# Performance work log

Measured on AMD Instinct MI355X. Metric: run time of the kernel, lower is better.

Reference implementation:

```python
import jax, jax.numpy as jnp
import numpy as np

WAY = 5
TEMPERATURE = 0.2
TEMPERATURE_ATTN = 5.0
BN_EPS = 1e-5


def bn_apply(x, p):
    # p: (4, C) = gamma, beta, running_mean, running_var (eval-mode BatchNorm)
    g, b, m, v = p[0], p[1], p[2], p[3]
    sh = (1, -1) + (1,) * (x.ndim - 2)
    return (x - m.reshape(sh)) * (g.reshape(sh) / jnp.sqrt(v.reshape(sh) + BN_EPS)) + b.reshape(sh)


def conv3d(x, w, pad):
    return jax.lax.conv_general_dilated(
        x, w, (1, 1, 1), [(pad[0], pad[0]), (pad[1], pad[1]), (pad[2], pad[2])],
        dimension_numbers=('NCDHW', 'OIDHW', 'NCDHW'))


def sepconv4d(x, conv2_w, bn2, conv1_w, bn1, proj_w, bnp):
    # x: (b, c, u, v, h, w). conv2: (k,k,1) kernel over (u,v); conv1: (1,k,k) over (h,w).
    b, c, u, v, h, w = x.shape
    y = x.reshape(b, c, u, v, h * w)
    y = bn_apply(conv3d(y, conv2_w, (1, 1, 0)), bn2)
    y = jax.nn.relu(y)
    y = y.reshape(b, c, u * v, h, w)
    y = bn_apply(conv3d(y, conv1_w, (0, 1, 1)), bn1)
    # 1x1 projection (pointwise over channels) + BN
    y = jnp.einsum('oc,bcxhw->boxhw', proj_w, y)
    y = bn_apply(y, bnp)
    return y.reshape(b, -1, u, v, h, w)


def cca(x, c1, c2):
    def branch(z):
        z = sepconv4d(z, *c1)
        z = jax.nn.relu(z)
        z = sepconv4d(z, *c2)
        return z
    perm = (0, 1, 4, 5, 2, 3)
    return branch(x) + jnp.transpose(branch(jnp.transpose(x, perm)), perm)


def gaussian_normalize(x, axis, eps=1e-5):
    m = jnp.mean(x, axis=axis, keepdims=True)
    v = jnp.var(x, axis=axis, keepdims=True, ddof=1)  # torch.var is unbiased
    return (x - m) / jnp.sqrt(v + eps)


def setup_inputs() -> dict:
    key = jax.random.key(0)
    ks = jax.random.split(key, 16)

    def bn_params(k, c):
        k1, k2, k3, k4 = jax.random.split(k, 4)
        g = 1.0 + 0.1 * jax.random.normal(k1, (c,), jnp.float32)
        b = 0.1 * jax.random.normal(k2, (c,), jnp.float32)
        m = 0.1 * jax.random.normal(k3, (c,), jnp.float32)
        v = 1.0 + 0.1 * jax.random.uniform(k4, (c,), jnp.float32)
        return jnp.stack([g, b, m, v])

    return {
        'spt': jax.random.normal(ks[0], (1, 5, 640, 10, 10), jnp.float32),
        'qry': jax.random.normal(ks[1], (75, 640, 10, 10), jnp.float32),
        'w_1x1': jax.random.normal(ks[2], (64, 640), jnp.float32) * 0.04,
        'bn_1x1': bn_params(ks[3], 64),
        'c1_conv2_w': jax.random.normal(ks[4], (1, 1, 3, 3, 1), jnp.float32) * 0.33,
        'c1_bn2': bn_params(ks[5], 1),
        'c1_conv1_w': jax.random.normal(ks[6], (1, 1, 1, 3, 3), jnp.float32) * 0.33,
        'c1_bn1': bn_params(ks[7], 1),
        'c1_proj_w': jax.random.normal(ks[8], (16, 1), jnp.float32),
        'c1_bnp': bn_params(ks[9], 16),
        'c2_conv2_w': jax.random.normal(ks[10], (16, 16, 3, 3, 1), jnp.float32) * 0.083,
        'c2_bn2': bn_params(ks[11], 16),
        'c2_conv1_w': jax.random.normal(ks[12], (16, 16, 1, 3, 3), jnp.float32) * 0.083,
        'c2_bn1': bn_params(ks[13], 16),
        'c2_proj_w': jax.random.normal(ks[14], (1, 16), jnp.float32) * 0.25,
        'c2_bnp': bn_params(ks[15], 1),
    }


def reference(spt, qry, w_1x1, bn_1x1,
              c1_conv2_w, c1_bn2, c1_conv1_w, c1_bn1, c1_proj_w, c1_bnp,
              c2_conv2_w, c2_bn2, c2_conv1_w, c2_bn1, c2_proj_w, c2_bnp):
    s = spt[0]                                   # (way, C, H, W)
    s = s - s.mean(axis=1, keepdims=True)        # normalize_feature
    q = qry - qry.mean(axis=1, keepdims=True)

    def cca1x1(x):
        y = jnp.einsum('oc,bchw->bohw', w_1x1, x)
        return jax.nn.relu(bn_apply(y, bn_1x1))

    sf = cca1x1(s)
    qf = cca1x1(q)
    sf = sf / jnp.maximum(jnp.linalg.norm(sf, axis=1, keepdims=True), 1e-8)
    qf = qf / jnp.maximum(jnp.linalg.norm(qf, axis=1, keepdims=True), 1e-8)

    # 4D correlation (avoids the repeat-induced 6D blowup of the original)
    corr = jnp.einsum('ncij,qckl->qnijkl', sf, qf)  # (Q, way, Hs, Ws, Hq, Wq)
    Q, way, Hs, Ws, Hq, Wq = corr.shape

    c1 = (c1_conv2_w, c1_bn2, c1_conv1_w, c1_bn1, c1_proj_w, c1_bnp)
    c2 = (c2_conv2_w, c2_bn2, c2_conv1_w, c2_bn1, c2_proj_w, c2_bnp)
    corr = cca(corr.reshape(Q * way, 1, Hs, Ws, Hq, Wq), c1, c2)

    corr_s = corr.reshape(Q, way, Hs * Ws, Hq, Wq)
    corr_q = corr.reshape(Q, way, Hs, Ws, Hq * Wq)
    corr_s = gaussian_normalize(corr_s, axis=2)
    corr_q = gaussian_normalize(corr_q, axis=4)
    corr_s = jax.nn.softmax(corr_s / TEMPERATURE_ATTN, axis=2).reshape(Q, way, Hs, Ws, Hq, Wq)
    corr_q = jax.nn.softmax(corr_q / TEMPERATURE_ATTN, axis=4).reshape(Q, way, Hs, Ws, Hq, Wq)

    attn_s = corr_s.sum(axis=(4, 5))             # (Q, way, Hs, Ws)
    attn_q = corr_q.sum(axis=(2, 3))             # (Q, way, Hq, Wq)

    spt_att = (attn_s[:, :, None] * s[None]).mean(axis=(-1, -2))       # (Q, way, C)
    qry_att = (attn_q[:, :, None] * q[:, None]).mean(axis=(-1, -2))    # (Q, way, C)
    qry_pooled = q.mean(axis=(-1, -2))                                  # (Q, C)

    num = jnp.sum(spt_att * qry_att, axis=-1)
    den = (jnp.maximum(jnp.linalg.norm(spt_att, axis=-1), 1e-8) *
           jnp.maximum(jnp.linalg.norm(qry_att, axis=-1), 1e-8))
    sim = (num / den) / TEMPERATURE
    return sim, qry_pooled
```

## Files before the change

kernel.cpp:

```cpp
#include <hip/hip_runtime.h>


#define NITEM 375

#define OFF_XTS 0
#define OFF_XTQ 160000
#define OFF_MP  2560000
#define OFF_SF  2568000
#define OFF_QF  2600000
#define OFF_RA  3080000
#define OFF_RB  6830000
#define OFF_PRM 10655000

#define PK2F 232
#define PK1F 1512
#define WSUMF 2792
#define SCVF 2856
#define SHVF 2920
#define PKWF 2984

#define Y1S2     20480
#define Y1GAP    1600
#define Y1HSTR   17600
#define Y1SSTR   35200
#define Y1BASE   (Y1S2 + Y1GAP)
#define ZPB2     127680
#define Y2S2     127712
#define Y2HALF2  16128
#define LDS_TOTAL2 159968

typedef float f4v __attribute__((ext_vector_type(4)));
typedef float f32x4 __attribute__((ext_vector_type(4)));
typedef _Float16 half8v __attribute__((ext_vector_type(8)));
typedef __fp16 fp16x2 __attribute__((ext_vector_type(2)));
typedef unsigned int u32x4 __attribute__((ext_vector_type(4)));
typedef unsigned int u32x2 __attribute__((ext_vector_type(2)));

__device__ __forceinline__ unsigned int pkrtz(float a, float b) {
  union { fp16x2 h; unsigned int u; } cv;
  cv.h = __builtin_amdgcn_cvt_pkrtz(a, b);
  return cv.u;
}

__global__ __launch_bounds__(256) void k_prep(
    const float* __restrict__ w1x1,  const float* __restrict__ bn1x1,
    const float* __restrict__ c1c2w, const float* __restrict__ c1bn2,
    const float* __restrict__ c1c1w, const float* __restrict__ c1bn1,
    const float* __restrict__ c1pj,  const float* __restrict__ c1bnp,
    const float* __restrict__ c2c2w, const float* __restrict__ c2bn2,
    const float* __restrict__ c2c1w, const float* __restrict__ c2bn1,
    const float* __restrict__ c2pj,  const float* __restrict__ c2bnp,
    float* __restrict__ prm)
{
  const int t = threadIdx.x;
  const float eps = 1e-5f;

  for (int idx = t; idx < 144; idx += 256) {
    int ds = idx / 16, i = idx % 16;
    float spv = c2bnp[0] / sqrtf(c2bnp[3] + eps);
    float acc = 0.f;
    for (int o = 0; o < 16; ++o) {
      float s1 = c2bn1[o] / sqrtf(c2bn1[48 + o] + eps);
      acc += c2pj[o] * s1 * c2c1w[(o * 16 + i) * 9 + ds];
    }
    prm[idx] = spv * acc;
  }
  for (int i = t; i < 16; i += 256) {
    float s = c1bnp[i] / sqrtf(c1bnp[48 + i] + eps);
    prm[144 + i] = s * c1pj[i];
    prm[160 + i] = c1bnp[16 + i] - c1bnp[32 + i] * s;
  }
  for (int o = t; o < 16; o += 256) {
    float s = c2bn2[o] / sqrtf(c2bn2[48 + o] + eps);
    prm[176 + o] = s;
    prm[192 + o] = c2bn2[16 + o] - c2bn2[32 + o] * s;
  }
  for (int k = t; k < 9; k += 256) {
    prm[208 + k] = c1c2w[k];
    prm[217 + k] = c1c1w[k];
  }
  if (t == 0) {
    float S2 = c1bn2[0] / sqrtf(c1bn2[3] + eps);
    prm[226] = S2;
    prm[227] = c1bn2[1] - c1bn2[2] * S2;
    float S1 = c1bn1[0] / sqrtf(c1bn1[3] + eps);
    prm[228] = S1;
    prm[229] = c1bn1[1] - c1bn1[2] * S1;
    float spv = c2bnp[0] / sqrtf(c2bnp[3] + eps);
    float k0 = 0.f;
    for (int o = 0; o < 16; ++o) {
      float s1 = c2bn1[o] / sqrtf(c2bn1[48 + o] + eps);
      k0 += c2pj[o] * (c2bn1[16 + o] - c2bn1[32 + o] * s1);
    }
    prm[230] = spv * (k0 - c2bnp[2]) + c2bnp[1];
    prm[231] = 0.f;
  }
  for (int o = t; o < 64; o += 256) {
    float s = 0.f;
    for (int c = 0; c < 640; ++c) s += w1x1[o * 640 + c];
    prm[WSUMF + o] = s;
    float scv = bn1x1[o] / sqrtf(bn1x1[192 + o] + eps);
    prm[SCVF + o] = scv;
    prm[SHVF + o] = bn1x1[64 + o] - bn1x1[128 + o] * scv;
  }
  __syncthreads();

  _Float16* pk2 = (_Float16*)(prm + PK2F);
  for (int idx = t; idx < 2560; idx += 256) {
    int c = idx >> 9, rem = idx & 511;
    int ln = rem >> 3, j = rem & 7;
    int o = ln & 15, qq = ln >> 4;
    int tap = 2 * c + (qq >> 1);
    int i = (qq & 1) * 8 + j;
    float v = (tap < 9) ? c2c2w[(o * 16 + i) * 9 + tap] : 0.f;
    pk2[idx] = (_Float16)v;
  }
  _Float16* pk1 = (_Float16*)(prm + PK1F);
  for (int idx = t; idx < 2560; idx += 256) {
    int c = idx >> 9, rem = idx & 511;
    int ln = rem >> 3, j = rem & 7;
    int m = ln & 15, qq = ln >> 4;
    int k = c * 32 + qq * 8 + j;
    int tp = k >> 4, i = k & 15;
    float v = (m == 0 && tp < 9) ? prm[tp * 16 + i] : 0.f;
    pk1[idx] = (_Float16)v;
  }
}

__global__ __launch_bounds__(256) void k_prepw(
    const float* __restrict__ w1x1, float* __restrict__ prm)
{
  _Float16* pkw = (_Float16*)(prm + PKWF);
  const int base = blockIdx.x * 800;
  for (int r = threadIdx.x; r < 800; r += 256) {
    int idx = base + r;
    int fi = idx >> 9, rem = idx & 511;
    int ln = rem >> 3, j = rem & 7;
    int cc = fi / 10, r2 = fi - cc * 10;
    int mt = r2 >> 1, kk = r2 & 1;
    int m = mt * 16 + (ln & 15);
    int k = cc * 64 + kk * 32 + ((ln >> 4) & 3) * 8 + j;
    float v = (m < 64) ? w1x1[m * 640 + k] : (m == 64 ? 1.f : 0.f);
    pkw[idx] = (_Float16)v;
  }
}

__global__ __launch_bounds__(512) void k_feat(
    const float* __restrict__ spt, const float* __restrict__ qry,
    float* __restrict__ ws, float* __restrict__ out)
{
  __shared__ __align__(16) _Float16 XTL[112 * 72];
  __shared__ __align__(16) float OUT[64 * 104];
  __shared__ __align__(16) float mrow[112];
  __shared__ __align__(16) float rn[112];
  __shared__ float CS[512];
  __shared__ float RS[640];
  __shared__ float msumL;

  const int b = blockIdx.x, t = threadIdx.x;
  const int lane = t & 63, wvv = t >> 6;
  const int n0 = lane & 15, qd = (lane >> 4) & 3;
  const float* src = (b < 5) ? spt + b * 64000 : qry + (b - 5) * 64000;
  float* dst = (b < 5) ? ws + OFF_SF + b * 6400 : ws + OFF_QF + (b - 5) * 6400;
  unsigned int* xtg = (unsigned int*)(ws + ((b < 5) ? (OFF_XTS + b * 32000)
                                                    : (OFF_XTQ + (b - 5) * 32000)));
  const float* prm = ws + OFF_PRM;
  const _Float16* pkw = (const _Float16*)(prm + PKWF);

  for (int idx = t; idx < 12 * 36; idx += 512)
    ((unsigned int*)(XTL + 100 * 72))[idx] = 0u;

  const int chp = t >> 3, part = t & 7;
  const int pLo = part * 13, pHi = (pLo + 13 < 100) ? pLo + 13 : 100;

  f32x4 acc[5];
  #pragma unroll
  for (int ti = 0; ti < 5; ++ti) { acc[ti][0]=0.f; acc[ti][1]=0.f; acc[ti][2]=0.f; acc[ti][3]=0.f; }

  for (int cc = 0; cc < 10; ++cc) {
    __syncthreads();
    for (int u = t; u < 800; u += 512) {
      int cp = u / 25, p4 = u - cp * 25;
      const float* r0 = src + (cc * 64 + 2 * cp) * 100 + p4 * 4;
      f4v a = *(const f4v*)r0;
      f4v c1 = *(const f4v*)(r0 + 100);
      #pragma unroll
      for (int e = 0; e < 4; ++e)
        *(unsigned int*)(XTL + (p4 * 4 + e) * 72 + 2 * cp) = pkrtz(a[e], c1[e]);
    }
    __syncthreads();
    for (int u = t; u < 3200; u += 512) {
      int p = u >> 5, cp = u & 31;
      xtg[p * 320 + cc * 32 + cp] = *(const unsigned int*)(XTL + p * 72 + 2 * cp);
    }
    #pragma unroll
    for (int kk = 0; kk < 2; ++kk) {
      #pragma unroll
      for (int ti = 0; ti < 5; ++ti) {
        int idx = wvv + ti * 8; if (idx > 34) idx = 34;
        int mt = idx / 7, nt = idx - mt * 7;
        half8v av = *(const half8v*)(pkw + (cc * 10 + mt * 2 + kk) * 512 + lane * 8);
        half8v bv = *(const half8v*)(XTL + (nt * 16 + n0) * 72 + kk * 32 + qd * 8);
        acc[ti] = __builtin_amdgcn_mfma_f32_16x16x32_f16(av, bv, acc[ti], 0, 0, 0);
      }
    }
    {
      float s = 0.f;
      for (int p = pLo; p < pHi; ++p) s += (float)XTL[p * 72 + chp];
      CS[t] = s;
    }
    __syncthreads();
    if (t < 64) {
      float s = 0.f;
      #pragma unroll
      for (int k = 0; k < 8; ++k) s += CS[t * 8 + k];
      RS[cc * 64 + t] = s;
    }
  }
  #pragma unroll
  for (int ti = 0; ti < 5; ++ti) {
    int idx = wvv + ti * 8; if (idx > 34) idx = 34;
    int mt = idx / 7, nt = idx - mt * 7;
    if (mt == 4 && qd == 0) {
      int p = nt * 16 + n0;
      mrow[p] = acc[ti][0] * (1.f / 640.f);
    }
  }
  __syncthreads();
  if (t == 0) { float s = 0.f; for (int p = 0; p < 100; ++p) s += mrow[p]; msumL = s; }
  #pragma unroll
  for (int ti = 0; ti < 5; ++ti) {
    int idx = wvv + ti * 8; if (idx > 34) idx = 34;
    int mt = idx / 7, nt = idx - mt * 7;
    if (mt < 4) {
      int p = nt * 16 + n0;
      if (p < 100) {
        float mp = mrow[p];
        #pragma unroll
        for (int r = 0; r < 4; ++r) {
          int o = mt * 16 + qd * 4 + r;
          float v = acc[ti][r] - prm[WSUMF + o] * mp;
          v = prm[SCVF + o] * v + prm[SHVF + o];
          OUT[o * 104 + p] = v > 0.f ? v : 0.f;
        }
      }
    }
  }
  __syncthreads();
  if (t < 100) {
    float s = 0.f;
    for (int o = 0; o < 64; ++o) { float v = OUT[o * 104 + t]; s += v * v; }
    float nr = sqrtf(s);
    rn[t] = 1.f / (nr > 1e-8f ? nr : 1e-8f);
    ws[OFF_MP + b * 100 + t] = mrow[t];
  }
  __syncthreads();
  for (int idx = t; idx < 1600; idx += 512) {
    int o = idx / 25, pq = idx - o * 25;
    f4v v = *(const f4v*)(OUT + o * 104 + pq * 4);
    f4v r4 = *(const f4v*)(rn + pq * 4);
    #pragma unroll
    for (int e = 0; e < 4; ++e) v[e] *= r4[e];
    *(f4v*)(dst + o * 100 + pq * 4) = v;
  }
  if (b >= 5) {
    const float msum = msumL;
    for (int gc = t; gc < 640; gc += 512)
      out[375 + (b - 5) * 640 + gc] = (RS[gc] - msum) * 0.01f;
  }
}

__global__ __launch_bounds__(1024) __attribute__((amdgpu_waves_per_eu(4, 4)))
void k_cca(float* __restrict__ ws)
{
  extern __shared__ char smem[];
  _Float16* T2h = (_Float16*)smem;
  float* sfL  = (float*)(smem + 20480);
  float* qfL  = (float*)(smem + 46080);
  float* CORR = (float*)(smem + 71680);
  float* T1   = (float*)(smem + 20480);

  const float* prm = ws + OFF_PRM;
  const int bid = blockIdx.x;
  const int it = bid >> 1, br = bid & 1;
  const int q = it / 5, n = it % 5;
  const int t = threadIdx.x;
  const int lane = t & 63, wv = t >> 6;
  const int n0 = lane & 15, qd = (lane >> 4) & 3;
  const int qh = qd >> 1, ih = qd & 1;

  const _Float16* pk2 = (const _Float16*)(prm + PK2F);
  const _Float16* pk1 = (const _Float16*)(prm + PK1F);
  half8v A2[5], A1[5];
  #pragma unroll
  for (int c = 0; c < 5; ++c) {
    A2[c] = *(const half8v*)(pk2 + c * 512 + lane * 8);
    A1[c] = *(const half8v*)(pk1 + c * 512 + lane * 8);
  }
  float sc2[4], bc2[4];
  #pragma unroll
  for (int r = 0; r < 4; ++r) { sc2[r] = prm[176 + qd * 4 + r]; bc2[r] = prm[192 + qd * 4 + r]; }

  const int d1E[5] = {-1,-1, 0, 0, 1}, d2E[5] = {-1, 1, 0,-1, 1};
  const int d1O[5] = {-1, 0, 0, 1, 0}, d2O[5] = { 0,-1, 1, 0, 0};

  int pp1[4], st1[4], addr2[4][5], posB[4];
  bool pv[4];
  #pragma unroll
  for (int ti = 0; ti < 4; ++ti) {
    int tile = wv + ti * 16; if (tile > 62) tile = 62;
    const int p = tile * 16 + n0;
    const int pcp = p < 1000 ? p : 999;
    pp1[ti] = pcp * 16;
    st1[ti] = Y2S2 + qh * Y2HALF2 + p * 16 + ih * 8;
    pv[ti] = (qd == 0) && (p < 1000);
    const int f2 = pcp / 100;
    const int s = pcp - f2 * 100;
    const int s1 = s / 10, s2 = s - s1 * 10;
    const bool rm = s1 > 0, rp = s1 < 9, cm = s2 > 0, cp2 = s2 < 9;
    const int b0 = Y2S2 + ih * Y2HALF2 + pcp * 16;
    #pragma unroll
    for (int c = 0; c < 5; ++c) {
      const bool vE = (d1E[c] < 0 ? rm : (d1E[c] > 0 ? rp : true)) &&
                      (d2E[c] < 0 ? cm : (d2E[c] > 0 ? cp2 : true));
      const bool vO = (c == 4) ? false :
                      ((d1O[c] < 0 ? rm : (d1O[c] > 0 ? rp : true)) &&
                       (d2O[c] < 0 ? cm : (d2O[c] > 0 ? cp2 : true)));
      const bool v = qh ? vO : vE;
      const int D1c = (qh ? (d1O[c] * 10 + d2O[c]) : (d1E[c] * 10 + d2E[c])) * 16;
      addr2[ti][c] = v ? (b0 + D1c) : ZPB2;
    }
    posB[ti] = br ? (s * 100 + f2) : (f2 * 100 + s);
  }
  const int posStride = br ? 10 : 1000;
  const int ihbase = Y1BASE + ih * Y1HSTR;

  {
    const f4v* sf4 = (const f4v*)(ws + OFF_SF + n * 6400);
    const f4v* qf4 = (const f4v*)(ws + OFF_QF + q * 6400);
    f4v* sL4 = (f4v*)sfL; f4v* qL4 = (f4v*)qfL;
    for (int idx = t; idx < 1600; idx += 1024) { sL4[idx] = sf4[idx]; qL4[idx] = qf4[idx]; }
  }
  __syncthreads();

  if (t < 625) {
    const int ij0 = (t / 25) * 4, kl0 = (t % 25) * 4;
    f4v acc4[4];
    #pragma unroll
    for (int jj = 0; jj < 4; ++jj) { acc4[jj][0]=0.f; acc4[jj][1]=0.f; acc4[jj][2]=0.f; acc4[jj][3]=0.f; }
    for (int c = 0; c < 64; ++c) {
      f4v sv = *(const f4v*)(sfL + c * 100 + ij0);
      f4v qv = *(const f4v*)(qfL + c * 100 + kl0);
      #pragma unroll
      for (int jj = 0; jj < 4; ++jj)
        #pragma unroll
        for (int e = 0; e < 4; ++e) acc4[jj][e] += sv[jj] * qv[e];
    }
    if (br == 0) {
      #pragma unroll
      for (int jj = 0; jj < 4; ++jj) *(f4v*)(CORR + (ij0 + jj) * 100 + kl0) = acc4[jj];
    } else {
      #pragma unroll
      for (int kk = 0; kk < 4; ++kk) {
        f4v tr;
        #pragma unroll
        for (int jj = 0; jj < 4; ++jj) tr[jj] = acc4[jj][kk];
        *(f4v*)(CORR + (kl0 + kk) * 100 + ij0) = tr;
      }
    }
  }
  __syncthreads();

  const float S2 = prm[226], B2 = prm[227], S1 = prm[228], B1 = prm[229];

  for (int idx = t; idx < 2500; idx += 1024) {
    int f = idx / 25, sq = (idx % 25) * 4;
    int f1 = f / 10, f2 = f - f1 * 10;
    f4v acc; acc[0]=0.f; acc[1]=0.f; acc[2]=0.f; acc[3]=0.f;
    #pragma unroll
    for (int du = 0; du < 3; ++du) {
      int nf1 = f1 + du - 1;
      if ((unsigned)nf1 >= 10u) continue;
      #pragma unroll
      for (int dv = 0; dv < 3; ++dv) {
        int nf2 = f2 + dv - 1;
        if ((unsigned)nf2 >= 10u) continue;
        float w = prm[208 + du * 3 + dv];
        f4v xv = *(const f4v*)(CORR + (nf1 * 10 + nf2) * 100 + sq);
        #pragma unroll
        for (int e = 0; e < 4; ++e) acc[e] += w * xv[e];
      }
    }
    #pragma unroll
    for (int e = 0; e < 4; ++e) { float v = S2 * acc[e] + B2; acc[e] = v > 0.f ? v : 0.f; }
    *(f4v*)(T1 + f * 100 + sq) = acc;
  }
  __syncthreads();

  if (t < 1000) {
    const int f = t / 10, s1 = t - (t / 10) * 10;
    const float* rowB = T1 + f * 100;
    f4v r[3][3];
    float w[3][3];
    #pragma unroll
    for (int dh = 0; dh < 3; ++dh) {
      int rr = s1 + dh - 1;
      bool okr = (unsigned)rr < 10u;
      int rc = rr < 0 ? 0 : (rr > 9 ? 9 : rr);
      const float* rp = rowB + rc * 10;
      r[dh][0] = *(const f4v*)(rp);
      r[dh][1] = *(const f4v*)(rp + 4);
      r[dh][2] = *(const f4v*)(rp + 8);
      #pragma unroll
      for (int dw = 0; dw < 3; ++dw) w[dh][dw] = okr ? prm[217 + dh * 3 + dw] : 0.f;
    }
    float o[10];
    #pragma unroll
    for (int s2 = 0; s2 < 10; ++s2) {
      float a = 0.f;
      #pragma unroll
      for (int dh = 0; dh < 3; ++dh)
        #pragma unroll
        for (int dw = 0; dw < 3; ++dw) {
          int col = s2 + dw - 1;
          if (col < 0 || col > 9) continue;
          a += w[dh][dw] * r[dh][col >> 2][col & 3];
        }
      o[s2] = a;
    }
    unsigned int* dst = (unsigned int*)((char*)T2h + (f * 100 + s1 * 10) * 2);
    #pragma unroll
    for (int k = 0; k < 5; ++k)
      dst[k] = pkrtz(S1 * o[2 * k] + B1, S1 * o[2 * k + 1] + B1);
  }
  __syncthreads();

  #define GEN_Y1(F1N)                                                          \
    if (t < 1000) {                                                            \
      const int _sl = (F1N) % 3;                                               \
      const float t2 = (float)T2h[(F1N) * 1000 + t];                           \
      unsigned int d[8];                                                       \
      _Pragma("unroll")                                                        \
      for (int j = 0; j < 8; ++j) {                                            \
        float ya = fmaxf(prm[144 + 2 * j] * t2 + prm[160 + 2 * j], 0.f);       \
        float yb = fmaxf(prm[145 + 2 * j] * t2 + prm[161 + 2 * j], 0.f);       \
        d[j] = pkrtz(ya, yb);                                                  \
      }                                                                        \
      u32x4 lo, hi;                                                            \
      lo[0]=d[0]; lo[1]=d[1]; lo[2]=d[2]; lo[3]=d[3];                          \
      hi[0]=d[4]; hi[1]=d[5]; hi[2]=d[6]; hi[3]=d[7];                          \
      *(u32x4*)(smem + Y1BASE + _sl * Y1SSTR + t * 16) = lo;                   \
      *(u32x4*)(smem + Y1BASE + _sl * Y1SSTR + Y1HSTR + t * 16) = hi;          \
    }

  GEN_Y1(0)
  GEN_Y1(1)
  {
    u32x4 zz; zz[0] = 0u; zz[1] = 0u; zz[2] = 0u; zz[3] = 0u;
    for (int idx = t; idx < 700; idx += 1024) {
      const int r = idx / 100;
      *(u32x4*)(smem + Y1S2 + r * Y1HSTR + (idx - r * 100) * 16) = zz;
    }
    for (int idx = t; idx < 2000; idx += 1024) {
      const int h = idx >= 1000 ? 1 : 0;
      *(u32x4*)(smem + Y1BASE + 2 * Y1SSTR + h * Y1HSTR + (idx - h * 1000) * 16) = zz;
    }
    if (t < 2) *(u32x4*)(smem + ZPB2 + t * 16) = zz;
  }
  __syncthreads();

  const float Cf = prm[230];
  float* resb = ws + (br ? OFF_RB : OFF_RA) + it * 10000;
  int gp = 0;

  for (int g = 0; g < 10; ++g) {
    const int o0 = (g % 3) * Y1SSTR;
    const int oP = ((g + 1) % 3) * Y1SSTR;
    const int oM = ((g + 2) % 3) * Y1SSTR;
    const int bM = ihbase + oM, b0s = ihbase + o0, bP = ihbase + oP;
    int base1[5];
    #pragma unroll
    for (int c = 0; c < 5; ++c) {
      const int eb = (d1E[c] < 0 ? bM : (d1E[c] > 0 ? bP : b0s)) + d2E[c] * 1600;
      const int ob = (d1O[c] < 0 ? bM : (d1O[c] > 0 ? bP : b0s)) + d2O[c] * 1600;
      base1[c] = qh ? ob : eb;
    }

    #pragma unroll
    for (int ti = 0; ti < 4; ++ti) {
      f32x4 acc; acc[0]=0.f; acc[1]=0.f; acc[2]=0.f; acc[3]=0.f;
      #pragma unroll
      for (int c = 0; c < 5; ++c) {
        half8v b = *(const half8v*)(smem + base1[c] + pp1[ti]);
        acc = __builtin_amdgcn_mfma_f32_16x16x32_f16(A2[c], b, acc, 0, 0, 0);
      }
      const float v0 = fmaxf(sc2[0] * acc[0] + bc2[0], 0.f);
      const float v1 = fmaxf(sc2[1] * acc[1] + bc2[1], 0.f);
      const float v2 = fmaxf(sc2[2] * acc[2] + bc2[2], 0.f);
      const float v3 = fmaxf(sc2[3] * acc[3] + bc2[3], 0.f);
      u32x2 wq; wq[0] = pkrtz(v0, v1); wq[1] = pkrtz(v2, v3);
      *(u32x2*)(smem + st1[ti]) = wq;
    }
    __syncthreads();

    #pragma unroll
    for (int ti = 0; ti < 4; ++ti) {
      f32x4 acc; acc[0]=0.f; acc[1]=0.f; acc[2]=0.f; acc[3]=0.f;
      #pragma unroll
      for (int c = 0; c < 5; ++c) {
        half8v b = *(const half8v*)(smem + addr2[ti][c]);
        acc = __builtin_amdgcn_mfma_f32_16x16x32_f16(A1[c], b, acc, 0, 0, 0);
      }
      if (pv[ti]) resb[posB[ti] + gp] = acc[0] + Cf;
    }
    if (g + 2 <= 9) { GEN_Y1(g + 2) }
    else if (g == 8) {
      u32x4 zz; zz[0] = 0u; zz[1] = 0u; zz[2] = 0u; zz[3] = 0u;
      for (int idx = t; idx < 2000; idx += 1024) {
        const int h = idx >= 1000 ? 1 : 0;
        *(u32x4*)(smem + Y1BASE + Y1SSTR + h * Y1HSTR + (idx - h * 1000) * 16) = zz;
      }
    }
    gp += posStride;
    __syncthreads();
  }
  #undef GEN_Y1
}

__global__ __launch_bounds__(256) void k_post(float* __restrict__ ws,
                                              float* __restrict__ out)
{
  __shared__ float F[10000];
  __shared__ float mc[100], ic[100], rc[100];
  __shared__ float mr[100], ir[100], rr[100];
  __shared__ float asL[100], aqL[100], msL[100], mqL[100];
  __shared__ float alph[2];
  __shared__ float red[12];
  const int it = blockIdx.x, t = threadIdx.x;
  const int q = it / 5, n = it % 5;

  const f4v* ra4 = (const f4v*)(ws + OFF_RA + it * 10000);
  const f4v* rb4 = (const f4v*)(ws + OFF_RB + it * 10000);
  f4v* F4 = (f4v*)F;
  for (int idx = t; idx < 2500; idx += 256) {
    f4v a = ra4[idx], b = rb4[idx];
    #pragma unroll
    for (int e = 0; e < 4; ++e) a[e] += b[e];
    F4[idx] = a;
  }
  if (t < 100) msL[t] = ws[OFF_MP + n * 100 + t];
  else if (t < 200) mqL[t - 100] = ws[OFF_MP + (5 + q) * 100 + t - 100];
  __syncthreads();

  if (t < 100) {
    float s = 0.f;
    for (int ij = 0; ij < 100; ++ij) s += F[ij * 100 + t];
    float m = s * 0.01f;
    float ss = 0.f;
    for (int ij = 0; ij < 100; ++ij) { float d = F[ij * 100 + t] - m; ss += d * d; }
    float inv = 1.f / (sqrtf(ss * (1.f / 99.f) + 1e-5f) * 5.f);
    float den = 0.f;
    for (int ij = 0; ij < 100; ++ij) den += __expf((F[ij * 100 + t] - m) * inv);
    mc[t] = m; ic[t] = inv; rc[t] = 1.f / den;
  } else if (t < 200) {
    const int r = t - 100;
    float s = 0.f;
    for (int kl = 0; kl < 100; ++kl) s += F[r * 100 + kl];
    float m = s * 0.01f;
    float ss = 0.f;
    for (int kl = 0; kl < 100; ++kl) { float d = F[r * 100 + kl] - m; ss += d * d; }
    float inv = 1.f / (sqrtf(ss * (1.f / 99.f) + 1e-5f) * 5.f);
    float den = 0.f;
    for (int kl = 0; kl < 100; ++kl) den += __expf((F[r * 100 + kl] - m) * inv);
    mr[r] = m; ir[r] = inv; rr[r] = 1.f / den;
  }
  __syncthreads();
  if (t < 100) {
    float s = 0.f;
    for (int kl = 0; kl < 100; ++kl)
      s += __expf((F[t * 100 + kl] - mc[kl]) * ic[kl]) * rc[kl];
    asL[t] = s;
  } else if (t < 200) {
    const int r = t - 100;
    float s2 = 0.f;
    for (int ij = 0; ij < 100; ++ij)
      s2 += __expf((F[ij * 100 + r] - mr[ij]) * ir[ij]) * rr[ij];
    aqL[r] = s2;
  }
  __syncthreads();
  if (t < 2) {
    float s = 0.f;
    for (int p = 0; p < 100; ++p) s += t ? (aqL[p] * mqL[p]) : (asL[p] * msL[p]);
    alph[t] = s;
  }
  __syncthreads();

  const unsigned int* xs = (const unsigned int*)(ws + OFF_XTS + n * 32000);
  const unsigned int* xq = (const unsigned int*)(ws + OFF_XTQ + q * 32000);
  const float als = alph[0], alq = alph[1];
  float dot = 0.f, na = 0.f, nb = 0.f;
  for (int u = t; u < 320; u += 256) {
    float s0 = 0.f, s1 = 0.f, q0 = 0.f, q1 = 0.f;
    for (int p = 0; p < 100; ++p) {
      union { unsigned int u; fp16x2 h; } a, bq;
      a.u = xs[p * 320 + u];
      bq.u = xq[p * 320 + u];
      float ap = asL[p], qp = aqL[p];
      s0 += ap * (float)a.h[0]; s1 += ap * (float)a.h[1];
      q0 += qp * (float)bq.h[0]; q1 += qp * (float)bq.h[1];
    }
    float sa0 = (s0 - als) * 0.01f, sa1 = (s1 - als) * 0.01f;
    float qa0 = (q0 - alq) * 0.01f, qa1 = (q1 - alq) * 0.01f;
    dot += sa0 * qa0 + sa1 * qa1;
    na  += sa0 * sa0 + sa1 * sa1;
    nb  += qa0 * qa0 + qa1 * qa1;
  }
  #pragma unroll
  for (int off = 32; off > 0; off >>= 1) {
    dot += __shfl_down(dot, off);
    na  += __shfl_down(na, off);
    nb  += __shfl_down(nb, off);
  }
  const int wid = t >> 6, lanei = t & 63;
  if (lanei == 0) { red[wid * 3 + 0] = dot; red[wid * 3 + 1] = na; red[wid * 3 + 2] = nb; }
  __syncthreads();
  if (t == 0) {
    dot = red[0] + red[3] + red[6] + red[9];
    na  = red[1] + red[4] + red[7] + red[10];
    nb  = red[2] + red[5] + red[8] + red[11];
    float ns = sqrtf(na); ns = ns > 1e-8f ? ns : 1e-8f;
    float nq2 = sqrtf(nb); nq2 = nq2 > 1e-8f ? nq2 : 1e-8f;
    out[it] = dot / (ns * nq2) * 5.f;
  }
}

extern "C" void kernel_launch(void* const* d_in, const int* in_sizes, int n_in,
                              void* d_out, int out_size, void* d_ws, size_t ws_size,
                              hipStream_t stream)
{
  (void)in_sizes; (void)n_in; (void)out_size; (void)ws_size;
  const float* spt    = (const float*)d_in[0];
  const float* qry    = (const float*)d_in[1];
  const float* w1x1   = (const float*)d_in[2];
  const float* bn1x1  = (const float*)d_in[3];
  const float* c1c2w  = (const float*)d_in[4];
  const float* c1bn2  = (const float*)d_in[5];
  const float* c1c1w  = (const float*)d_in[6];
  const float* c1bn1  = (const float*)d_in[7];
  const float* c1pj   = (const float*)d_in[8];
  const float* c1bnp  = (const float*)d_in[9];
  const float* c2c2w  = (const float*)d_in[10];
  const float* c2bn2  = (const float*)d_in[11];
  const float* c2c1w  = (const float*)d_in[12];
  const float* c2bn1  = (const float*)d_in[13];
  const float* c2pj   = (const float*)d_in[14];
  const float* c2bnp  = (const float*)d_in[15];
  float* ws  = (float*)d_ws;
  float* out = (float*)d_out;

  k_prep<<<1, 256, 0, stream>>>(w1x1, bn1x1,
                                c1c2w, c1bn2, c1c1w, c1bn1, c1pj, c1bnp,
                                c2c2w, c2bn2, c2c1w, c2bn1, c2pj, c2bnp,
                                ws + OFF_PRM);
  k_prepw<<<64, 256, 0, stream>>>(w1x1, ws + OFF_PRM);
  k_feat<<<80, 512, 0, stream>>>(spt, qry, ws, out);

  (void)hipFuncSetAttribute((const void*)k_cca,
                            hipFuncAttributeMaxDynamicSharedMemorySize, LDS_TOTAL2);
  k_cca<<<NITEM * 2, 1024, LDS_TOTAL2, stream>>>(ws);

  k_post<<<NITEM, 256, 0, stream>>>(ws, out);
}
```

Measured before the change: 340.2 us.

## Double-buffer feature staging, parallelize weight sums, interleave CCA LDS halves

k_feat now double-buffers the fp16 transposed tile in shared memory, prefetching the next channel chunk into registers while the current one feeds MFMA. This removes one barrier per iteration and hides global load latency. The w1x1 row sums and BN folding move from a serial loop in the single-block k_prep into the 64-block k_prepw, using a wave-shuffle reduction. The k_cca LDS layout interleaves the two channel halves per position (32-byte stride) instead of keeping separate half-planes, which changes bank access patterns and adds slightly more LDS.

```diff
diff --git a/kernel.cpp b/kernel.cpp
--- a/kernel.cpp
+++ b/kernel.cpp
@@ -19,15 +19,12 @@
 #define SHVF 2920
 #define PKWF 2984
 
-#define Y1S2     20480
-#define Y1GAP    1600
-#define Y1HSTR   17600
-#define Y1SSTR   35200
-#define Y1BASE   (Y1S2 + Y1GAP)
-#define ZPB2     127680
-#define Y2S2     127712
-#define Y2HALF2  16128
-#define LDS_TOTAL2 159968
+#define Y1SLOT0  23680
+#define Y1GAP3   3200
+#define Y1SSTR3  35200
+#define ZPB3     20480
+#define Y2S3     129280
+#define LDS_TOTAL3 161536
 
 typedef float f4v __attribute__((ext_vector_type(4)));
 typedef float f32x4 __attribute__((ext_vector_type(4)));
@@ -52,6 +49,7 @@
     const float* __restrict__ c2pj,  const float* __restrict__ c2bnp,
     float* __restrict__ prm)
 {
+  (void)w1x1; (void)bn1x1;
   const int t = threadIdx.x;
   const float eps = 1e-5f;
 
@@ -95,14 +93,6 @@
     prm[230] = spv * (k0 - c2bnp[2]) + c2bnp[1];
     prm[231] = 0.f;
   }
-  for (int o = t; o < 64; o += 256) {
-    float s = 0.f;
-    for (int c = 0; c < 640; ++c) s += w1x1[o * 640 + c];
-    prm[WSUMF + o] = s;
-    float scv = bn1x1[o] / sqrtf(bn1x1[192 + o] + eps);
-    prm[SCVF + o] = scv;
-    prm[SHVF + o] = bn1x1[64 + o] - bn1x1[128 + o] * scv;
-  }
   __syncthreads();
 
   _Float16* pk2 = (_Float16*)(prm + PK2F);
@@ -128,11 +118,14 @@
 }
 
 __global__ __launch_bounds__(256) void k_prepw(
-    const float* __restrict__ w1x1, float* __restrict__ prm)
+    const float* __restrict__ w1x1, const float* __restrict__ bn1x1,
+    float* __restrict__ prm)
 {
+  __shared__ float red[4];
   _Float16* pkw = (_Float16*)(prm + PKWF);
+  const int t = threadIdx.x;
   const int base = blockIdx.x * 800;
-  for (int r = threadIdx.x; r < 800; r += 256) {
+  for (int r = t; r < 800; r += 256) {
     int idx = base + r;
     int fi = idx >> 9, rem = idx & 511;
     int ln = rem >> 3, j = rem & 7;
@@ -143,17 +136,29 @@
     float v = (m < 64) ? w1x1[m * 640 + k] : (m == 64 ? 1.f : 0.f);
     pkw[idx] = (_Float16)v;
   }
+  const int o = blockIdx.x;
+  float s = 0.f;
+  for (int c = t; c < 640; c += 256) s += w1x1[o * 640 + c];
+  #pragma unroll
+  for (int off = 32; off > 0; off >>= 1) s += __shfl_down(s, off);
+  if ((t & 63) == 0) red[t >> 6] = s;
+  __syncthreads();
+  if (t == 0) {
+    prm[WSUMF + o] = red[0] + red[1] + red[2] + red[3];
+    float scv = bn1x1[o] / sqrtf(bn1x1[192 + o] + 1e-5f);
+    prm[SCVF + o] = scv;
+    prm[SHVF + o] = bn1x1[64 + o] - bn1x1[128 + o] * scv;
+  }
 }
 
 __global__ __launch_bounds__(512) void k_feat(
     const float* __restrict__ spt, const float* __restrict__ qry,
     float* __restrict__ ws, float* __restrict__ out)
 {
-  __shared__ __align__(16) _Float16 XTL[112 * 72];
-  __shared__ __align__(16) float OUT[64 * 104];
+  __shared__ __align__(16) char POOL[2 * 16128];
   __shared__ __align__(16) float mrow[112];
   __shared__ __align__(16) float rn[112];
-  __shared__ float CS[512];
+  __shared__ float CS[2][512];
   __shared__ float RS[640];
   __shared__ float msumL;
 
@@ -167,8 +172,20 @@
   const float* prm = ws + OFF_PRM;
   const _Float16* pkw = (const _Float16*)(prm + PKWF);
 
-  for (int idx = t; idx < 12 * 36; idx += 512)
-    ((unsigned int*)(XTL + 100 * 72))[idx] = 0u;
+  for (int idx = t; idx < 864; idx += 512) {
+    int bsel = idx / 432, r = idx - bsel * 432;
+    ((unsigned int*)(POOL + bsel * 16128 + 100 * 144))[r] = 0u;
+  }
+  for (int u = t; u < 800; u += 512) {
+    int cp = u / 25, p4 = u - cp * 25;
+    const float* r0 = src + (2 * cp) * 100 + p4 * 4;
+    f4v a = *(const f4v*)r0;
+    f4v c1 = *(const f4v*)(r0 + 100);
+    #pragma unroll
+    for (int e = 0; e < 4; ++e)
+      *(unsigned int*)((_Float16*)POOL + (p4 * 4 + e) * 72 + 2 * cp) = pkrtz(a[e], c1[e]);
+  }
+  __syncthreads();
 
   const int chp = t >> 3, part = t & 7;
   const int pLo = part * 13, pHi = (pLo + 13 < 100) ? pLo + 13 : 100;
@@ -178,20 +195,26 @@
   for (int ti = 0; ti < 5; ++ti) { acc[ti][0]=0.f; acc[ti][1]=0.f; acc[ti][2]=0.f; acc[ti][3]=0.f; }
 
   for (int cc = 0; cc < 10; ++cc) {
-    __syncthreads();
-    for (int u = t; u < 800; u += 512) {
-      int cp = u / 25, p4 = u - cp * 25;
-      const float* r0 = src + (cc * 64 + 2 * cp) * 100 + p4 * 4;
-      f4v a = *(const f4v*)r0;
-      f4v c1 = *(const f4v*)(r0 + 100);
-      #pragma unroll
-      for (int e = 0; e < 4; ++e)
-        *(unsigned int*)(XTL + (p4 * 4 + e) * 72 + 2 * cp) = pkrtz(a[e], c1[e]);
-    }
-    __syncthreads();
+    const int cur = cc & 1;
+    const _Float16* Xc = (const _Float16*)(POOL + cur * 16128);
+    _Float16* Xn = (_Float16*)(POOL + (cur ^ 1) * 16128);
+
+    f4v pa[2], pc[2];
+    if (cc < 9) {
+      #pragma unroll
+      for (int k = 0; k < 2; ++k) {
+        int u = t + k * 512;
+        if (u < 800) {
+          int cp = u / 25, p4 = u - cp * 25;
+          const float* r0 = src + ((cc + 1) * 64 + 2 * cp) * 100 + p4 * 4;
+          pa[k] = *(const f4v*)r0;
+          pc[k] = *(const f4v*)(r0 + 100);
+        }
+      }
+    }
     for (int u = t; u < 3200; u += 512) {
       int p = u >> 5, cp = u & 31;
-      xtg[p * 320 + cc * 32 + cp] = *(const unsigned int*)(XTL + p * 72 + 2 * cp);
+      xtg[p * 320 + cc * 32 + cp] = *(const unsigned int*)(Xc + p * 72 + 2 * cp);
     }
     #pragma unroll
     for (int kk = 0; kk < 2; ++kk) {
@@ -200,20 +223,32 @@
         int idx = wvv + ti * 8; if (idx > 34) idx = 34;
         int mt = idx / 7, nt = idx - mt * 7;
         half8v av = *(const half8v*)(pkw + (cc * 10 + mt * 2 + kk) * 512 + lane * 8);
-        half8v bv = *(const half8v*)(XTL + (nt * 16 + n0) * 72 + kk * 32 + qd * 8);
+        half8v bv = *(const half8v*)(Xc + (nt * 16 + n0) * 72 + kk * 32 + qd * 8);
         acc[ti] = __builtin_amdgcn_mfma_f32_16x16x32_f16(av, bv, acc[ti], 0, 0, 0);
       }
     }
     {
       float s = 0.f;
-      for (int p = pLo; p < pHi; ++p) s += (float)XTL[p * 72 + chp];
-      CS[t] = s;
+      for (int p = pLo; p < pHi; ++p) s += (float)Xc[p * 72 + chp];
+      CS[cur][t] = s;
+    }
+    if (cc < 9) {
+      #pragma unroll
+      for (int k = 0; k < 2; ++k) {
+        int u = t + k * 512;
+        if (u < 800) {
+          int cp = u / 25, p4 = u - cp * 25;
+          #pragma unroll
+          for (int e = 0; e < 4; ++e)
+            *(unsigned int*)(Xn + (p4 * 4 + e) * 72 + 2 * cp) = pkrtz(pa[k][e], pc[k][e]);
+        }
+      }
     }
     __syncthreads();
     if (t < 64) {
       float s = 0.f;
       #pragma unroll
-      for (int k = 0; k < 8; ++k) s += CS[t * 8 + k];
+      for (int k = 0; k < 8; ++k) s += CS[cur][t * 8 + k];
       RS[cc * 64 + t] = s;
     }
   }
@@ -227,6 +262,7 @@
     }
   }
   __syncthreads();
+  float* OUT = (float*)POOL;
   if (t == 0) { float s = 0.f; for (int p = 0; p < 100; ++p) s += mrow[p]; msumL = s; }
   #pragma unroll
   for (int ti = 0; ti < 5; ++ti) {
@@ -311,14 +347,14 @@
     int tile = wv + ti * 16; if (tile > 62) tile = 62;
     const int p = tile * 16 + n0;
     const int pcp = p < 1000 ? p : 999;
-    pp1[ti] = pcp * 16;
-    st1[ti] = Y2S2 + qh * Y2HALF2 + p * 16 + ih * 8;
+    pp1[ti] = pcp * 32 + ih * 16;
+    st1[ti] = Y2S3 + p * 32 + qh * 16 + ih * 8;
     pv[ti] = (qd == 0) && (p < 1000);
     const int f2 = pcp / 100;
     const int s = pcp - f2 * 100;
     const int s1 = s / 10, s2 = s - s1 * 10;
     const bool rm = s1 > 0, rp = s1 < 9, cm = s2 > 0, cp2 = s2 < 9;
-    const int b0 = Y2S2 + ih * Y2HALF2 + pcp * 16;
+    const int b0 = Y2S3 + pcp * 32 + ih * 16;
     #pragma unroll
     for (int c = 0; c < 5; ++c) {
       const bool vE = (d1E[c] < 0 ? rm : (d1E[c] > 0 ? rp : true)) &&
@@ -327,13 +363,12 @@
                       ((d1O[c] < 0 ? rm : (d1O[c] > 0 ? rp : true)) &&
                        (d2O[c] < 0 ? cm : (d2O[c] > 0 ? cp2 : true)));
       const bool v = qh ? vO : vE;
-      const int D1c = (qh ? (d1O[c] * 10 + d2O[c]) : (d1E[c] * 10 + d2E[c])) * 16;
-      addr2[ti][c] = v ? (b0 + D1c) : ZPB2;
+      const int D1c = (qh ? (d1O[c] * 10 + d2O[c]) : (d1E[c] * 10 + d2E[c]));
+      addr2[ti][c] = v ? (b0 + D1c * 32) : ZPB3;
     }
     posB[ti] = br ? (s * 100 + f2) : (f2 * 100 + s);
   }
   const int posStride = br ? 10 : 1000;
-  const int ihbase = Y1BASE + ih * Y1HSTR;
 
   {
     const f4v* sf4 = (const f4v*)(ws + OFF_SF + n * 6400);
@@ -449,23 +484,20 @@
       u32x4 lo, hi;                                                            \
       lo[0]=d[0]; lo[1]=d[1]; lo[2]=d[2]; lo[3]=d[3];                          \
       hi[0]=d[4]; hi[1]=d[5]; hi[2]=d[6]; hi[3]=d[7];                          \
-      *(u32x4*)(smem + Y1BASE + _sl * Y1SSTR + t * 16) = lo;                   \
-      *(u32x4*)(smem + Y1BASE + _sl * Y1SSTR + Y1HSTR + t * 16) = hi;          \
+      *(u32x4*)(smem + Y1SLOT0 + _sl * Y1SSTR3 + t * 32) = lo;                 \
+      *(u32x4*)(smem + Y1SLOT0 + _sl * Y1SSTR3 + t * 32 + 16) = hi;            \
     }
 
   GEN_Y1(0)
   GEN_Y1(1)
   {
     u32x4 zz; zz[0] = 0u; zz[1] = 0u; zz[2] = 0u; zz[3] = 0u;
-    for (int idx = t; idx < 700; idx += 1024) {
-      const int r = idx / 100;
-      *(u32x4*)(smem + Y1S2 + r * Y1HSTR + (idx - r * 100) * 16) = zz;
-    }
-    for (int idx = t; idx < 2000; idx += 1024) {
-      const int h = idx >= 1000 ? 1 : 0;
-      *(u32x4*)(smem + Y1BASE + 2 * Y1SSTR + h * Y1HSTR + (idx - h * 1000) * 16) = zz;
-    }
-    if (t < 2) *(u32x4*)(smem + ZPB2 + t * 16) = zz;
+    for (int idx = t; idx < 800; idx += 1024) {
+      const int r = idx / 200;
+      *(u32x4*)(smem + 20480 + r * Y1SSTR3 + (idx - r * 200) * 16) = zz;
+    }
+    for (int idx = t; idx < 2000; idx += 1024)
+      *(u32x4*)(smem + Y1SLOT0 + 2 * Y1SSTR3 + idx * 16) = zz;
   }
   __syncthreads();
 
@@ -474,16 +506,15 @@
   int gp = 0;
 
   for (int g = 0; g < 10; ++g) {
-    const int o0 = (g % 3) * Y1SSTR;
-    const int oP = ((g + 1) % 3) * Y1SSTR;
-    const int oM = ((g + 2) % 3) * Y1SSTR;
-    const int bM = ihbase + oM, b0s = ihbase + o0, bP = ihbase + oP;
+    const int o0 = (g % 3) * Y1SSTR3;
+    const int oP = ((g + 1) % 3) * Y1SSTR3;
+    const int oM = ((g + 2) % 3) * Y1SSTR3;
     int base1[5];
     #pragma unroll
     for (int c = 0; c < 5; ++c) {
-      const int eb = (d1E[c] < 0 ? bM : (d1E[c] > 0 ? bP : b0s)) + d2E[c] * 1600;
-      const int ob = (d1O[c] < 0 ? bM : (d1O[c] > 0 ? bP : b0s)) + d2O[c] * 1600;
-      base1[c] = qh ? ob : eb;
+      const int eb = (d1E[c] < 0 ? oM : (d1E[c] > 0 ? oP : o0)) + d2E[c] * 3200;
+      const int ob = (d1O[c] < 0 ? oM : (d1O[c] > 0 ? oP : o0)) + d2O[c] * 3200;
+      base1[c] = Y1SLOT0 + (qh ? ob : eb);
     }
 
     #pragma unroll
@@ -516,10 +547,8 @@
     if (g + 2 <= 9) { GEN_Y1(g + 2) }
     else if (g == 8) {
       u32x4 zz; zz[0] = 0u; zz[1] = 0u; zz[2] = 0u; zz[3] = 0u;
-      for (int idx = t; idx < 2000; idx += 1024) {
-        const int h = idx >= 1000 ? 1 : 0;
-        *(u32x4*)(smem + Y1BASE + Y1SSTR + h * Y1HSTR + (idx - h * 1000) * 16) = zz;
-      }
+      for (int idx = t; idx < 2000; idx += 1024)
+        *(u32x4*)(smem + Y1SLOT0 + Y1SSTR3 + idx * 16) = zz;
     }
     gp += posStride;
     __syncthreads();
@@ -662,12 +691,12 @@
                                 c1c2w, c1bn2, c1c1w, c1bn1, c1pj, c1bnp,
                                 c2c2w, c2bn2, c2c1w, c2bn1, c2pj, c2bnp,
                                 ws + OFF_PRM);
-  k_prepw<<<64, 256, 0, stream>>>(w1x1, ws + OFF_PRM);
+  k_prepw<<<64, 256, 0, stream>>>(w1x1, bn1x1, ws + OFF_PRM);
   k_feat<<<80, 512, 0, stream>>>(spt, qry, ws, out);
 
   (void)hipFuncSetAttribute((const void*)k_cca,
-                            hipFuncAttributeMaxDynamicSharedMemorySize, LDS_TOTAL2);
-  k_cca<<<NITEM * 2, 1024, LDS_TOTAL2, stream>>>(ws);
+                            hipFuncAttributeMaxDynamicSharedMemorySize, LDS_TOTAL3);
+  k_cca<<<NITEM * 2, 1024, LDS_TOTAL3, stream>>>(ws);
 
   k_post<<<NITEM, 256, 0, stream>>>(ws, out);
 }
```

Result: faster. 329.0 us (-3.3%).
